# Kernel tuning notes

Hardware: AMD Instinct MI355X
Metric: run time of the kernel (lower is better)

## Reference

```python
import jax, jax.numpy as jnp
import numpy as np
import math

SEQ_LEN = 720
PRED_LEN = 720
CHANNELS = 862
BATCH = 64
IN_LEN = SEQ_LEN // 2  # seq_len is even -> no padding branch


def dct2_ortho_matrix(N):
    # Orthonormal DCT-II matrix D so that dct(x, norm='ortho') = x @ D.T along last axis
    n = jnp.arange(N, dtype=jnp.float32)
    k = n[:, None]
    D = jnp.cos(jnp.pi * (n[None, :] + 0.5) * k / N) * jnp.sqrt(2.0 / N)
    D = D.at[0].multiply(1.0 / jnp.sqrt(2.0))
    return D  # [N, N], row k = frequency k


def setup_inputs() -> dict:
    key = jax.random.key(0)
    ks = jax.random.split(key, 7)
    x = jax.random.normal(ks[0], (BATCH, SEQ_LEN, CHANNELS), dtype=jnp.float32)
    # depthwise 1x1 convs == per-channel scale + bias
    w1 = jax.random.normal(ks[1], (CHANNELS,), dtype=jnp.float32) * 0.1
    b1 = jax.random.normal(ks[2], (CHANNELS,), dtype=jnp.float32) * 0.1
    w2 = jax.random.normal(ks[3], (CHANNELS,), dtype=jnp.float32) * 0.1
    b2 = jax.random.normal(ks[4], (CHANNELS,), dtype=jnp.float32) * 0.1
    # Linear(in_len, pred_len): W [pred_len, in_len], b [pred_len]
    W_lo = jax.random.normal(ks[5], (PRED_LEN, IN_LEN), dtype=jnp.float32) / math.sqrt(IN_LEN)
    b_lo = jax.random.normal(ks[6], (PRED_LEN,), dtype=jnp.float32) * 0.01
    return {"x": x, "w1": w1, "b1": b1, "w2": w2, "b2": b2, "W_lo": W_lo, "b_lo": b_lo}


def reference(x, w1, b1, w2, b2, W_lo, b_lo):
    B, L, C = x.shape
    xt = jnp.transpose(x, (0, 2, 1))              # [B, C, L]
    seq_mean = jnp.mean(xt, axis=-1, keepdims=True)
    xt = xt - seq_mean
    # depthwise low-pass conv, kernel [1,1]/sqrt(2), stride 2
    lp = xt.reshape(B, C, L // 2, 2).sum(-1) / jnp.sqrt(jnp.float32(2.0))  # [B, C, N]
    N = L // 2
    D = dct2_ortho_matrix(N)
    xd = jnp.einsum('bcn,kn->bck', lp, D) / N     # DCT-II ortho along last axis, scaled
    # x += conv1x1_1(conv1x1_2(x)) -- depthwise 1x1 convs are per-channel affine
    y = (xd * w2[:, None] + b2[:, None]) * w1[:, None] + b1[:, None]
    xd = xd + y
    out = jnp.einsum('bcn,pn->bcp', xd, W_lo) + b_lo  # Linear(in_len -> pred_len)
    out = out + seq_mean                           # [B, C, pred_len]
    return jnp.transpose(out, (0, 2, 1))           # [B, pred_len, C]
```

## Files before the change

### kernel.cpp

```cpp
#include <hip/hip_runtime.h>
#include <hip/hip_bf16.h>
#include <cstdint>

#define SEQ   720
#define PRED  720
#define CH    862
#define NB    64
#define NIN   360
#define KP    384
#define CP    896
#define PP    768
#define BK    32

typedef __attribute__((ext_vector_type(8))) short s16x8;
typedef __attribute__((ext_vector_type(4))) float f32x4;
typedef __attribute__((ext_vector_type(2))) float f32x2;
typedef unsigned int u32;
typedef unsigned short u16;

__device__ __forceinline__ u16 to_bf16u(float f){
  __hip_bfloat16 h = __float2bfloat16(f);
  return *reinterpret_cast<u16*>(&h);
}

__global__ __launch_bounds__(256) void k_prep0(const float* __restrict__ Wlo,
                                               u16* __restrict__ Dt, u16* __restrict__ Wbf,
                                               float* __restrict__ Srow, float* __restrict__ Slo){
  int bid = blockIdx.x, t = threadIdx.x;
  if (bid < 576){
    int idx = bid*256 + t;
    int m = idx / 384, n = idx % 384;
    u16 v = 0;
    if (m < NIN && n < NIN){
      int r = ((2*m+1)*n) % (4*NIN);
      float ang = (float)r * (float)(3.14159265358979323846 / 720.0);
      float x = cosf(ang) * 0.07453559924999299f;
      if (n == 0) x *= 0.7071067811865476f;
      v = to_bf16u(x);
    }
    Dt[idx] = v;
  } else if (bid < 1728){
    int idx = (bid - 576)*256 + t;
    int p = idx / 384, n = idx % 384;
    u16 v = 0;
    if (p < PRED && n < NIN) v = to_bf16u(Wlo[(size_t)p*NIN + n]);
    Wbf[idx] = v;
  } else {
    int w = t >> 6, l = t & 63;
    int p = (bid - 1728)*4 + w;
    if (p < PRED){
      const float* row = Wlo + (size_t)p*NIN;
      float s = 0.f;
      for (int i = l; i < NIN; i += 64) s += row[i];
      #pragma unroll
      for (int off = 32; off > 0; off >>= 1) s += __shfl_down(s, off);
      if (l == 0){
        Slo[p]  = s;
        Srow[p] = row[0] * 0.05270462766947299f;
      }
    }
  }
}

#define GLOAD_LDS16(gp, lp_) __builtin_amdgcn_global_load_lds( \
    (const __attribute__((address_space(1))) u32*)(gp), \
    (__attribute__((address_space(3))) u32*)(lp_), 16, 0, 0)

__global__ __launch_bounds__(256, 4) void k_mgemm(const u16* __restrict__ Wbf, const u16* __restrict__ Dt,
                                                  u16* __restrict__ Mbf){
  int bid = blockIdx.x;
  int pt = bid % 6;
  int mt = bid / 6;

  int t  = threadIdx.x;
  int w  = t >> 6, l = t & 63;
  int wr = w >> 1, wc = w & 1;

  __shared__ __align__(16) char smem[32768];
  u16 (*As)[128*BK] = reinterpret_cast<u16(*)[128*BK]>(smem);
  u16 (*Bs)[128*BK] = reinterpret_cast<u16(*)[128*BK]>(smem + 16384);
  float (*wb2)[132] = reinterpret_cast<float(*)[132]>(smem);

  f32x4 acc[4][4] = {};

  const u16* Abase = Wbf + (size_t)pt*128*KP;
  const u16* Bbase = Dt + (size_t)mt*128*KP;
  int srow = t >> 2;
  int squad = t & 3;
  int row16 = l & 15, kb = l >> 4;
  int sperm = (srow >> 1) & 3;
  int rperm = (row16 >> 1) & 3;

#define STAGEM(bufi, k0) do { \
    GLOAD_LDS16(Abase + (size_t)(srow)*KP + (k0) + ((squad^sperm))*8,      &As[bufi][(srow)*BK + squad*8]); \
    GLOAD_LDS16(Abase + (size_t)(64 + srow)*KP + (k0) + ((squad^sperm))*8, &As[bufi][(64 + srow)*BK + squad*8]); \
    GLOAD_LDS16(Bbase + (size_t)(srow)*KP + (k0) + ((squad^sperm))*8,      &Bs[bufi][(srow)*BK + squad*8]); \
    GLOAD_LDS16(Bbase + (size_t)(64 + srow)*KP + (k0) + ((squad^sperm))*8, &Bs[bufi][(64 + srow)*BK + squad*8]); \
  } while(0)

  STAGEM(0, 0);
  for (int ks = 0; ks < 12; ks++){
    int cur = ks & 1;
    if (ks < 11){
      STAGEM(cur ^ 1, (ks + 1) * BK);
      asm volatile("s_waitcnt vmcnt(4)" ::: "memory");
    } else {
      asm volatile("s_waitcnt vmcnt(0)" ::: "memory");
    }
    __builtin_amdgcn_s_barrier();
    const u16* aB = &As[cur][(wr*64 + row16)*BK + (kb^rperm)*8];
    const u16* bB = &Bs[cur][(wc*64 + row16)*BK + (kb^rperm)*8];
    s16x8 bfr[4];
    #pragma unroll
    for (int ni = 0; ni < 4; ni++)
      bfr[ni] = *reinterpret_cast<const s16x8*>(bB + ni*16*BK);
    #pragma unroll
    for (int mi = 0; mi < 4; mi++){
      s16x8 af = *reinterpret_cast<const s16x8*>(aB + mi*16*BK);
      #pragma unroll
      for (int ni = 0; ni < 4; ni++)
        acc[mi][ni] = __builtin_amdgcn_mfma_f32_16x16x32_bf16(af, bfr[ni], acc[mi][ni], 0, 0, 0);
    }
    __builtin_amdgcn_s_barrier();
  }
  __syncthreads();

  const float inv360 = 1.0f/360.0f;
  #pragma unroll 1
  for (int mi = 0; mi < 4; mi++){
    #pragma unroll
    for (int ni = 0; ni < 4; ni++)
      #pragma unroll
      for (int r = 0; r < 4; r++)
        wb2[wr*16 + kb*4 + r][wc*64 + ni*16 + row16] = acc[mi][ni][r];
    __syncthreads();
    #pragma unroll
    for (int it = 0; it < 2; it++){
      int wi = it*256 + t;
      int rl = wi >> 4, seg = wi & 15;
      int p = pt*128 + (rl>>4)*64 + mi*16 + (rl & 15);
      f32x4 g0 = *reinterpret_cast<const f32x4*>(&wb2[rl][seg*8]);
      f32x4 g1 = *reinterpret_cast<const f32x4*>(&wb2[rl][seg*8 + 4]);
      uint4 pk;
      pk.x = (u32)to_bf16u(g0.x*inv360) | ((u32)to_bf16u(g0.y*inv360) << 16);
      pk.y = (u32)to_bf16u(g0.z*inv360) | ((u32)to_bf16u(g0.w*inv360) << 16);
      pk.z = (u32)to_bf16u(g1.x*inv360) | ((u32)to_bf16u(g1.y*inv360) << 16);
      pk.w = (u32)to_bf16u(g1.z*inv360) | ((u32)to_bf16u(g1.w*inv360) << 16);
      *reinterpret_cast<uint4*>(&Mbf[(size_t)p*KP + mt*128 + seg*8]) = pk;
    }
    __syncthreads();
  }
}

__global__ __launch_bounds__(256) void k_pre(const float* __restrict__ x, u16* __restrict__ pairB,
                                             float* __restrict__ meanw){
  int b  = blockIdx.y;
  int c0 = blockIdx.x * 64;
  int t  = threadIdx.x;
  int c16  = t & 15;
  int mrow = t >> 4;
  int w    = t >> 6;
  __shared__ u16  pl[192][66];
  __shared__ float red[4][64];
  const float rs2 = 0.7071067811865476f;
  int cb = c0 + c16*4;
  bool full = (cb + 3 < CH);
  const float* xb = x + (size_t)b*SEQ*CH + cb;
  float s0=0.f, s1=0.f, s2=0.f, s3=0.f;
  int rowc = t >> 2;
  int mq0  = t & 3;
  size_t rbase = ((size_t)b*CP + c0 + rowc) * KP;

  #pragma unroll 1
  for (int h = 0; h < 2; h++){
    #pragma unroll 1
    for (int ml = mrow; ml < 192; ml += 16){
      int m = h*192 + ml;
      float p0=0.f, p1=0.f, p2=0.f, p3=0.f;
      if (m < NIN){
        const float* r0 = xb + (size_t)(2*m)*CH;
        float a0,a1,a2,a3, e0,e1,e2,e3;
        if (full){
          f32x4 va = *reinterpret_cast<const f32x4*>(r0);
          f32x2 vb = *reinterpret_cast<const f32x2*>(r0 + CH);
          f32x2 vc = *reinterpret_cast<const f32x2*>(r0 + CH + 2);
          a0=va.x; a1=va.y; a2=va.z; a3=va.w;
          e0=vb.x; e1=vb.y; e2=vc.x; e3=vc.y;
        } else {
          a0 = (cb+0<CH)? r0[0]:0.f; a1 = (cb+1<CH)? r0[1]:0.f;
          a2 = (cb+2<CH)? r0[2]:0.f; a3 = (cb+3<CH)? r0[3]:0.f;
          e0 = (cb+0<CH)? r0[CH+0]:0.f; e1 = (cb+1<CH)? r0[CH+1]:0.f;
          e2 = (cb+2<CH)? r0[CH+2]:0.f; e3 = (cb+3<CH)? r0[CH+3]:0.f;
        }
        p0=a0+e0; p1=a1+e1; p2=a2+e2; p3=a3+e3;
        s0+=p0; s1+=p1; s2+=p2; s3+=p3;
      }
      u32 lo = (u32)to_bf16u(p0*rs2) | ((u32)to_bf16u(p1*rs2) << 16);
      u32 hi = (u32)to_bf16u(p2*rs2) | ((u32)to_bf16u(p3*rs2) << 16);
      *reinterpret_cast<u32*>(&pl[ml][c16*4 + 0]) = lo;
      *reinterpret_cast<u32*>(&pl[ml][c16*4 + 2]) = hi;
    }
    __syncthreads();
    #pragma unroll
    for (int i = 0; i < 6; i++){
      int mg = mq0 + 4*i;
      u16 vals[8];
      #pragma unroll
      for (int j = 0; j < 8; j++) vals[j] = pl[mg*8 + j][rowc];
      uint4 pk;
      pk.x = (u32)vals[0] | ((u32)vals[1] << 16);
      pk.y = (u32)vals[2] | ((u32)vals[3] << 16);
      pk.z = (u32)vals[4] | ((u32)vals[5] << 16);
      pk.w = (u32)vals[6] | ((u32)vals[7] << 16);
      *reinterpret_cast<uint4*>(pairB + rbase + h*192 + (size_t)mg*8) = pk;
    }
    __syncthreads();
  }

  s0 += __shfl_down(s0, 32); s1 += __shfl_down(s1, 32);
  s2 += __shfl_down(s2, 32); s3 += __shfl_down(s3, 32);
  s0 += __shfl_down(s0, 16); s1 += __shfl_down(s1, 16);
  s2 += __shfl_down(s2, 16); s3 += __shfl_down(s3, 16);
  if ((t & 63) < 16){
    f32x4 rv; rv.x=s0; rv.y=s1; rv.z=s2; rv.w=s3;
    *reinterpret_cast<f32x4*>(&red[w][c16*4]) = rv;
  }
  __syncthreads();
  if (t < 64){
    float mean = (red[0][t] + red[1][t] + red[2][t] + red[3][t]) * (1.0f/SEQ);
    meanw[(size_t)b*CP + c0 + t] = mean;
  }
}

__global__ __launch_bounds__(256, 4) void k_gemm(const u16* __restrict__ Apack, const u16* __restrict__ Mbf,
                                              const float* __restrict__ Srow, const float* __restrict__ Slo,
                                              const float* __restrict__ meanw,
                                              const float* __restrict__ w1, const float* __restrict__ b1,
                                              const float* __restrict__ w2, const float* __restrict__ b2,
                                              const float* __restrict__ blo,
                                              float* __restrict__ out){
  int bid = blockIdx.x;
  int idx = (bid & 7) * 336 + (bid >> 3);
  int pt  = idx % 6;
  int rem = idx / 6;
  int ct  = rem % 7;
  int b   = rem / 7;

  int t  = threadIdx.x;
  int w  = t >> 6, l = t & 63;
  int wr = w >> 1, wc = w & 1;

  __shared__ __align__(16) char smem[32768];
  u16 (*As)[128*BK] = reinterpret_cast<u16(*)[128*BK]>(smem);
  u16 (*Bs)[128*BK] = reinterpret_cast<u16(*)[128*BK]>(smem + 16384);
  float (*wbuf)[16][132] = reinterpret_cast<float(*)[16][132]>(smem);

  f32x4 acc[4][4] = {};

  const u16* Abase = Apack + ((size_t)b*CP + (size_t)ct*128) * KP;
  const u16* Bbase = Mbf + (size_t)pt*128*KP;
  int srow = t >> 2;
  int squad = t & 3;
  int row16 = l & 15, kb = l >> 4;
  int sperm = (srow >> 1) & 3;
  int rperm = (row16 >> 1) & 3;

#define STAGE(bufi, k0) do { \
    GLOAD_LDS16(Abase + (size_t)(srow)*KP + (k0) + ((squad^sperm))*8,      &As[bufi][(srow)*BK + squad*8]); \
    GLOAD_LDS16(Abase + (size_t)(64 + srow)*KP + (k0) + ((squad^sperm))*8, &As[bufi][(64 + srow)*BK + squad*8]); \
    GLOAD_LDS16(Bbase + (size_t)(srow)*KP + (k0) + ((squad^sperm))*8,      &Bs[bufi][(srow)*BK + squad*8]); \
    GLOAD_LDS16(Bbase + (size_t)(64 + srow)*KP + (k0) + ((squad^sperm))*8, &Bs[bufi][(64 + srow)*BK + squad*8]); \
  } while(0)

  STAGE(0, 0);
  for (int ks = 0; ks < 12; ks++){
    int cur = ks & 1;
    if (ks < 11){
      STAGE(cur ^ 1, (ks + 1) * BK);
      asm volatile("s_waitcnt vmcnt(4)" ::: "memory");
    } else {
      asm volatile("s_waitcnt vmcnt(0)" ::: "memory");
    }
    __builtin_amdgcn_s_barrier();
    const u16* aB = &As[cur][(wr*64 + row16)*BK + (kb^rperm)*8];
    const u16* bB = &Bs[cur][(wc*64 + row16)*BK + (kb^rperm)*8];
    s16x8 bfr[4];
    #pragma unroll
    for (int ni = 0; ni < 4; ni++)
      bfr[ni] = *reinterpret_cast<const s16x8*>(bB + ni*16*BK);
    __builtin_amdgcn_s_setprio(1);
    #pragma unroll
    for (int mi = 0; mi < 4; mi++){
      s16x8 af = *reinterpret_cast<const s16x8*>(aB + mi*16*BK);
      #pragma unroll
      for (int ni = 0; ni < 4; ni++)
        acc[mi][ni] = __builtin_amdgcn_mfma_f32_16x16x32_bf16(af, bfr[ni], acc[mi][ni], 0, 0, 0);
    }
    __builtin_amdgcn_s_setprio(0);
    __builtin_amdgcn_s_barrier();
  }
  __syncthreads();

  int c32 = t & 31;
  int cb4 = ct*128 + c32*4;
  float sc4[4], of4[4], cn4[4], bc4[4];
  #pragma unroll
  for (int j = 0; j < 4; j++){
    int c = cb4 + j;
    bool v = (c < CH);
    float w1v = v ? w1[c] : 0.f, w2v = v ? w2[c] : 0.f;
    float b1v = v ? b1[c] : 0.f, b2v = v ? b2[c] : 0.f;
    float mv  = v ? meanw[(size_t)b*CP + c] : 0.f;
    sc4[j] = 1.f + w1v*w2v;
    of4[j] = w1v*b2v + b1v;
    cn4[j] = mv;
    bc4[j] = 1.4142135623730951f * sc4[j] * mv;
  }
  bool cfull = (cb4 + 3 < CH);
  size_t outb = (size_t)b*PRED*CH;
  int prow = t >> 5;

  #pragma unroll
  for (int ni = 0; ni < 4; ni++){
    #pragma unroll
    for (int mi = 0; mi < 4; mi++)
      #pragma unroll
      for (int r = 0; r < 4; r++)
        wbuf[wc][row16][wr*64 + mi*16 + kb*4 + r] = acc[mi][ni][r];
    __syncthreads();
    #pragma unroll
    for (int k = 0; k < 4; k++){
      int wcp   = k >> 1;
      int p_loc = (k & 1)*8 + prow;
      int p = pt*128 + wcp*64 + ni*16 + p_loc;
      if (p < PRED){
        f32x4 g = *reinterpret_cast<const f32x4*>(&wbuf[wcp][p_loc][c32*4]);
        float sp = Srow[p], sl = Slo[p], bl = blo[p];
        f32x4 ov;
        #pragma unroll
        for (int j = 0; j < 4; j++)
          ov[j] = sc4[j]*g[j] + (cn4[j] - bc4[j]*sp + of4[j]*sl + bl);
        float* op = &out[outb + (size_t)p*CH + cb4];
        if (cfull){
          *reinterpret_cast<f32x4*>(op) = ov;
        } else {
          #pragma unroll
          for (int j = 0; j < 4; j++)
            if (cb4 + j < CH) op[j] = ov[j];
        }
      }
    }
    __syncthreads();
  }
}

extern "C" void kernel_launch(void* const* d_in, const int* in_sizes, int n_in,
                              void* d_out, int out_size, void* d_ws, size_t ws_size,
                              hipStream_t stream)
{
  const float* x   = (const float*)d_in[0];
  const float* w1  = (const float*)d_in[1];
  const float* b1  = (const float*)d_in[2];
  const float* w2  = (const float*)d_in[3];
  const float* b2  = (const float*)d_in[4];
  const float* Wlo = (const float*)d_in[5];
  const float* blo = (const float*)d_in[6];
  float* out = (float*)d_out;

  char* ws = (char*)d_ws;
  u16*   Dt    = (u16*)(ws);
  u16*   Wbf   = (u16*)(ws + 294912);
  u16*   Mbf   = (u16*)(ws + 884736);
  float* Srow  = (float*)(ws + 1474560);
  float* Slo   = (float*)(ws + 1477632);
  u16*   pairB = (u16*)(ws + 1480704);
  float* meanw = (float*)(ws + 45520896);

  k_prep0<<<dim3(1908), dim3(256), 0, stream>>>(Wlo, Dt, Wbf, Srow, Slo);
  k_mgemm<<<dim3(18), dim3(256), 0, stream>>>(Wbf, Dt, Mbf);
  k_pre<<<dim3(CP/64, NB), dim3(256), 0, stream>>>(x, pairB, meanw);
  k_gemm<<<dim3(6*7*NB), dim3(256), 0, stream>>>(pairB, Mbf, Srow, Slo, meanw,
                                                 w1, b1, w2, b2, blo, out);
}
```

Baseline: 154.7 us.

## Split GEMM epilogue into separate output kernel via bf16 intermediate buffer

The GEMM kernel no longer applies the per-channel affine, mean and bias epilogue or writes the strided output. It stores its raw accumulator tiles as bf16 into a workspace buffer G. A new k_out kernel reads G and writes full output rows across all channels, with the aim of more contiguous stores. This adds an extra kernel launch, a write and re-read of the intermediate (about 88 MB), and an extra bf16 rounding of the GEMM results, which costs accuracy.

```diff
diff --git a/kernel.cpp b/kernel.cpp
--- a/kernel.cpp
+++ b/kernel.cpp
@@ -21,6 +21,10 @@
 __device__ __forceinline__ u16 to_bf16u(float f){
   __hip_bfloat16 h = __float2bfloat16(f);
   return *reinterpret_cast<u16*>(&h);
+}
+__device__ __forceinline__ float from_bf16u(u16 u){
+  u32 w = ((u32)u) << 16;
+  return *reinterpret_cast<float*>(&w);
 }
 
 __global__ __launch_bounds__(256) void k_prep0(const float* __restrict__ Wlo,
@@ -233,12 +237,7 @@
 }
 
 __global__ __launch_bounds__(256, 4) void k_gemm(const u16* __restrict__ Apack, const u16* __restrict__ Mbf,
-                                              const float* __restrict__ Srow, const float* __restrict__ Slo,
-                                              const float* __restrict__ meanw,
-                                              const float* __restrict__ w1, const float* __restrict__ b1,
-                                              const float* __restrict__ w2, const float* __restrict__ b2,
-                                              const float* __restrict__ blo,
-                                              float* __restrict__ out){
+                                                 u16* __restrict__ G){
   int bid = blockIdx.x;
   int idx = (bid & 7) * 336 + (bid >> 3);
   int pt  = idx % 6;
@@ -301,23 +300,8 @@
   }
   __syncthreads();
 
+  size_t gbase = (((size_t)b*6 + pt)*7 + ct) * (size_t)(128*128);
   int c32 = t & 31;
-  int cb4 = ct*128 + c32*4;
-  float sc4[4], of4[4], cn4[4], bc4[4];
-  #pragma unroll
-  for (int j = 0; j < 4; j++){
-    int c = cb4 + j;
-    bool v = (c < CH);
-    float w1v = v ? w1[c] : 0.f, w2v = v ? w2[c] : 0.f;
-    float b1v = v ? b1[c] : 0.f, b2v = v ? b2[c] : 0.f;
-    float mv  = v ? meanw[(size_t)b*CP + c] : 0.f;
-    sc4[j] = 1.f + w1v*w2v;
-    of4[j] = w1v*b2v + b1v;
-    cn4[j] = mv;
-    bc4[j] = 1.4142135623730951f * sc4[j] * mv;
-  }
-  bool cfull = (cb4 + 3 < CH);
-  size_t outb = (size_t)b*PRED*CH;
   int prow = t >> 5;
 
   #pragma unroll
@@ -332,25 +316,82 @@
     for (int k = 0; k < 4; k++){
       int wcp   = k >> 1;
       int p_loc = (k & 1)*8 + prow;
-      int p = pt*128 + wcp*64 + ni*16 + p_loc;
-      if (p < PRED){
-        f32x4 g = *reinterpret_cast<const f32x4*>(&wbuf[wcp][p_loc][c32*4]);
-        float sp = Srow[p], sl = Slo[p], bl = blo[p];
-        f32x4 ov;
+      int prow_g = wcp*64 + ni*16 + p_loc;
+      f32x4 g = *reinterpret_cast<const f32x4*>(&wbuf[wcp][p_loc][c32*4]);
+      uint2 pk;
+      pk.x = (u32)to_bf16u(g.x) | ((u32)to_bf16u(g.y) << 16);
+      pk.y = (u32)to_bf16u(g.z) | ((u32)to_bf16u(g.w) << 16);
+      *reinterpret_cast<uint2*>(&G[gbase + (size_t)prow_g*128 + c32*4]) = pk;
+    }
+    __syncthreads();
+  }
+}
+
+__global__ __launch_bounds__(256) void k_out(const u16* __restrict__ G,
+                                             const float* __restrict__ Srow, const float* __restrict__ Slo,
+                                             const float* __restrict__ meanw,
+                                             const float* __restrict__ w1, const float* __restrict__ b1,
+                                             const float* __restrict__ w2, const float* __restrict__ b2,
+                                             const float* __restrict__ blo,
+                                             float* __restrict__ out){
+  int bid = blockIdx.x;
+  int half = bid & 1;
+  int pt   = (bid >> 1) % 6;
+  int b    = bid / 12;
+  int t = threadIdx.x;
+  int w = t >> 6, l = t & 63;
+
+  const u16* gb = G + (((size_t)b*6 + pt)*7) * (size_t)(128*128);
+  size_t outb = (size_t)b*PRED*CH;
+  const float rt2 = 1.4142135623730951f;
+
+  #pragma unroll 1
+  for (int i = 0; i < 4; i++){
+    int c = l*4 + i*256;
+    if (c >= 896) continue;
+    int ctc = c >> 7, cl = c & 127;
+    const u16* gchunk = gb + (size_t)ctc*(128*128) + cl;
+    float sc4[4], of4[4], mv4[4];
+    bool cfull = (c + 3 < CH);
+    #pragma unroll
+    for (int j = 0; j < 4; j++){
+      int cc = (c + j < CH) ? (c + j) : (CH - 1);
+      float w1v = w1[cc], w2v = w2[cc];
+      sc4[j] = 1.f + w1v*w2v;
+      of4[j] = w1v*b2[cc] + b1[cc];
+      mv4[j] = meanw[(size_t)b*CP + c + j];
+    }
+    float cn4[4], bc4[4];
+    #pragma unroll
+    for (int j = 0; j < 4; j++){
+      cn4[j] = mv4[j];
+      bc4[j] = rt2 * sc4[j] * mv4[j];
+    }
+    #pragma unroll 1
+    for (int rr = 0; rr < 16; rr++){
+      int p_loc = half*64 + w*16 + rr;
+      int p = pt*128 + p_loc;
+      if (p >= PRED) continue;
+      uint2 gp = *reinterpret_cast<const uint2*>(gchunk + (size_t)p_loc*128);
+      float g0 = from_bf16u((u16)(gp.x & 0xffff)), g1 = from_bf16u((u16)(gp.x >> 16));
+      float g2 = from_bf16u((u16)(gp.y & 0xffff)), g3 = from_bf16u((u16)(gp.y >> 16));
+      float sp = Srow[p], sl = Slo[p], bl = blo[p];
+      float base0 = -0.f;
+      f32x4 ov;
+      ov.x = sc4[0]*g0 + (cn4[0] - bc4[0]*sp + of4[0]*sl + bl);
+      ov.y = sc4[1]*g1 + (cn4[1] - bc4[1]*sp + of4[1]*sl + bl);
+      ov.z = sc4[2]*g2 + (cn4[2] - bc4[2]*sp + of4[2]*sl + bl);
+      ov.w = sc4[3]*g3 + (cn4[3] - bc4[3]*sp + of4[3]*sl + bl);
+      (void)base0;
+      float* op = &out[outb + (size_t)p*CH + c];
+      if (cfull){
+        *reinterpret_cast<f32x4*>(op) = ov;
+      } else {
         #pragma unroll
         for (int j = 0; j < 4; j++)
-          ov[j] = sc4[j]*g[j] + (cn4[j] - bc4[j]*sp + of4[j]*sl + bl);
-        float* op = &out[outb + (size_t)p*CH + cb4];
-        if (cfull){
-          *reinterpret_cast<f32x4*>(op) = ov;
-        } else {
-          #pragma unroll
-          for (int j = 0; j < 4; j++)
-            if (cb4 + j < CH) op[j] = ov[j];
-        }
+          if (c + j < CH) op[j] = ov[j];
       }
     }
-    __syncthreads();
   }
 }
 
@@ -375,10 +416,11 @@
   float* Slo   = (float*)(ws + 1477632);
   u16*   pairB = (u16*)(ws + 1480704);
   float* meanw = (float*)(ws + 45520896);
+  u16*   G     = (u16*)(ws + 45750272);
 
   k_prep0<<<dim3(1908), dim3(256), 0, stream>>>(Wlo, Dt, Wbf, Srow, Slo);
   k_mgemm<<<dim3(18), dim3(256), 0, stream>>>(Wbf, Dt, Mbf);
   k_pre<<<dim3(CP/64, NB), dim3(256), 0, stream>>>(x, pairB, meanw);
-  k_gemm<<<dim3(6*7*NB), dim3(256), 0, stream>>>(pairB, Mbf, Srow, Slo, meanw,
-                                                 w1, b1, w2, b2, blo, out);
-}
+  k_gemm<<<dim3(6*7*NB), dim3(256), 0, stream>>>(pairB, Mbf, G);
+  k_out<<<dim3(NB*6*2), dim3(256), 0, stream>>>(G, Srow, Slo, meanw, w1, b1, w2, b2, blo, out);
+}
```

New measurement: 208.0 us. 34.5% more time.
